# Kernel optimization log

Measured on AMD Instinct MI355X. Metric: run time of the kernel, lower is better.

The kernel has to match this reference:

```python
import jax, jax.numpy as jnp
import numpy as np

N_USERS = 8192
D = 128
E = 262144        # known edges (nonzero_idx rows)
K = 131072        # static pad size for data-dependent candidate extraction
COS_THR = 0.3
TAU = 0.2


def setup_inputs() -> dict:
    key = jax.random.key(0)
    k1, k2, k3, k4 = jax.random.split(key, 4)
    user_emb = jax.random.normal(k1, (N_USERS, D), dtype=jnp.float32)
    nonzero_idx = jax.random.randint(k2, (E, 2), 0, N_USERS)
    W = jax.random.normal(k3, (2, 2 * D), dtype=jnp.float32) * 0.05  # mlp_s weight [2, 2*latent]
    b = jnp.zeros((2,), dtype=jnp.float32)                            # mlp_s bias
    gumbel_noise = jax.random.gumbel(k4, (E + K, 2), dtype=jnp.float32)
    return {"user_emb": user_emb, "W": W, "b": b,
            "gumbel_noise": gumbel_noise, "nonzero_idx": nonzero_idx}


def reference(user_emb, W, b, gumbel_noise, nonzero_idx):
    n = user_emb.shape[0]
    # ---- get_candidate_pair ----
    norm = jnp.linalg.norm(user_emb, axis=1, keepdims=True)
    u = user_emb / jnp.maximum(norm, 1e-12)          # F.normalize(dim=1)
    cos = u @ u.T                                    # [n, n]
    diag = jnp.arange(n)
    cos = cos.at[diag, diag].set(-1.0)               # fill_diagonal_(-1)
    cos = cos.at[nonzero_idx[:, 0], nonzero_idx[:, 1]].set(-1.0)
    mask = cos > COS_THR
    # static-size nonzero; padded slots point at (0,0) where cos == -1,
    # so they behave as invalid candidates (weight 0 downstream).
    ci, cj = jnp.nonzero(mask, size=K, fill_value=0)
    cand_vals = cos[ci, cj]                          # padded entries = -1
    cand_idx = jnp.stack([ci, cj], axis=1)           # [K, 2]

    # ---- forward ----
    pair_idx = jnp.concatenate([nonzero_idx, cand_idx], axis=0)   # [E+K, 2]
    u_emb = user_emb[pair_idx[:, 0]]
    v_emb = user_emb[pair_idx[:, 1]]
    concat_emb = jnp.concatenate([u_emb, v_emb], axis=1)          # [E+K, 2D]
    logits = concat_emb @ W.T + b                                 # [E+K, 2]

    # hard gumbel-softmax (straight-through)
    y_soft = jax.nn.softmax((logits + gumbel_noise) / TAU, axis=-1)
    y_hard = jax.nn.one_hot(jnp.argmax(y_soft, axis=-1), 2, dtype=y_soft.dtype)
    gumbel_output = y_hard + y_soft - jax.lax.stop_gradient(y_soft)
    gumbel_retain = gumbel_output[:, 0]                           # [E+K]

    # ---- get_edge_weight ----
    cand_w = jnp.maximum(cand_vals, 0.0)                          # masked_fill(<0, 0)
    weights = jnp.concatenate([jnp.ones((E,), dtype=cand_w.dtype), cand_w])
    w = gumbel_retain * weights                                   # [E+K]
    gumbel_01 = w
    gumbel_retain_w = jnp.concatenate([w[:, None], w[:, None]], axis=0)  # [2(E+K), 1]
    return gumbel_01, gumbel_retain_w, pair_idx
```

## Files before the change

kernel.cpp:

```cpp
#include <hip/hip_runtime.h>
#include <hip/hip_bf16.h>
#include <math.h>

#define N_USERS 8192
#define DIMS    128
#define EDGES   262144
#define KCAND   131072
#define NTOT    (EDGES + KCAND)
#define LISTCAP 131072
#define CAPB    512
#define NTILES  2080
#define COS_THR 0.3f
#define EPS_SEL 6e-3f
#define LOGIT_MARGIN 2e-3f
#define DEADKEY 0xFFFFFFFFu

typedef short bf16x8 __attribute__((ext_vector_type(8)));
typedef float f32x4  __attribute__((ext_vector_type(4)));


__global__ __launch_bounds__(256) void prep_k(const float* __restrict__ x,
                                              const float* __restrict__ W,
                                              const int* __restrict__ nz,
                                              float* __restrict__ un,
                                              unsigned short* __restrict__ u0,
                                              float4* __restrict__ P,
                                              unsigned* __restrict__ excl) {
  if (blockIdx.x < 256) {
#pragma clang fp contract(off)
    const int tid  = threadIdx.x;
    const int rloc = tid >> 3;
    const int j    = tid & 7;
    const int i    = blockIdx.x * 32 + rloc;
    const float* r = x + (size_t)i * DIMS;

    float vals[16];
    float a = 0.f;
#pragma unroll
    for (int b8 = 0; b8 < 16; ++b8) {
      float t = r[b8 * 8 + j];
      vals[b8] = t;
      a = a + t * t;
    }
    a = a + __shfl_xor(a, 1, 64);
    a = a + __shfl_xor(a, 2, 64);
    float s = a + __shfl_xor(a, 4, 64);
    float n = (float)sqrt((double)s);
    n = fmaxf(n, 1e-12f);

    unsigned short* slab = u0 + (size_t)(i >> 7) * 16384 + (i & 127) * 8;
    float p0 = 0.f, p1 = 0.f, p2 = 0.f, p3 = 0.f;
#pragma unroll
    for (int b8 = 0; b8 < 16; ++b8) {
      int k = b8 * 8 + j;
      float t = vals[b8];
      float v = t / n;
      un[(size_t)i * DIMS + k] = v;
      __hip_bfloat16 h = __float2bfloat16(v);
      slab[(size_t)b8 * 1024 + j] = *(unsigned short*)&h;
      p0 = fmaf(t, W[k], p0);
      p1 = fmaf(t, W[128 + k], p1);
      p2 = fmaf(t, W[256 + k], p2);
      p3 = fmaf(t, W[384 + k], p3);
    }
#pragma unroll
    for (int m = 1; m < 8; m <<= 1) {
      p0 += __shfl_xor(p0, m, 64);
      p1 += __shfl_xor(p1, m, 64);
      p2 += __shfl_xor(p2, m, 64);
      p3 += __shfl_xor(p3, m, 64);
    }
    if (j == 0) P[i] = make_float4(p0, p1, p2, p3);
  } else {
    int t = (blockIdx.x - 256) * 256 + threadIdx.x;
    if (t < EDGES) {
      uint2 e = ((const uint2*)nz)[t];
      atomicOr(&excl[(size_t)e.x * 256 + (e.y >> 5)], 1u << (e.y & 31));
    }
  }
}

__global__ __launch_bounds__(512) void mfma_pass(const unsigned short* __restrict__ u0,
                                                 uint2* __restrict__ list,
                                                 int* __restrict__ gcount) {
  __shared__ uint2 svec[CAPB];
  __shared__ int lcnt, lbase;

  const int tid  = threadIdx.x;
  const int lane = tid & 63;
  const int wv   = tid >> 6;
  const int quad = lane >> 4;
  const int l15  = lane & 15;

  int rem = blockIdx.x, bi = 0;
  while (rem >= 64 - bi) { rem -= 64 - bi; ++bi; }
  const int bj = bi + rem;
  const int I0 = bi * 128, J0 = bj * 128;
  const int moff = (wv & 3) * 32, noff = (wv >> 2) * 64;

  if (tid == 0) lcnt = 0;
  __syncthreads();

  const unsigned short* __restrict__ Abase = u0 + (size_t)bi * 16384;
  const unsigned short* __restrict__ Bbase = u0 + (size_t)bj * 16384;

  bf16x8 af[4][2], bfr[4][4];
#pragma unroll
  for (int kc = 0; kc < 4; ++kc) {
    const int cq = kc * 4 + quad;
#pragma unroll
    for (int mt = 0; mt < 2; ++mt)
      af[kc][mt] = *(const bf16x8*)&Abase[(size_t)(cq * 128 + moff + mt * 16 + l15) * 8];
#pragma unroll
    for (int nt = 0; nt < 4; ++nt)
      bfr[kc][nt] = *(const bf16x8*)&Bbase[(size_t)(cq * 128 + noff + nt * 16 + l15) * 8];
  }

  f32x4 acc[2][4];
#pragma unroll
  for (int mt = 0; mt < 2; ++mt)
#pragma unroll
    for (int nt = 0; nt < 4; ++nt)
#pragma unroll
      for (int g = 0; g < 4; ++g) acc[mt][nt][g] = 0.f;

#pragma unroll
  for (int kc = 0; kc < 4; ++kc)
#pragma unroll
    for (int mt = 0; mt < 2; ++mt)
#pragma unroll
      for (int nt = 0; nt < 4; ++nt)
        acc[mt][nt] = __builtin_amdgcn_mfma_f32_16x16x32_bf16(
            af[kc][mt], bfr[kc][nt], acc[mt][nt], 0, 0, 0);

#pragma unroll
  for (int mt = 0; mt < 2; ++mt)
#pragma unroll
    for (int nt = 0; nt < 4; ++nt)
#pragma unroll
      for (int g = 0; g < 4; ++g) {
        float v = acc[mt][nt][g];
        if (v > COS_THR - EPS_SEL) {
          int i = I0 + moff + mt * 16 + quad * 4 + g;
          int j = J0 + noff + nt * 16 + l15;
          if (j > i) {
            int idx = atomicAdd(&lcnt, 2);
            if (idx + 1 < CAPB) {
              svec[idx]     = make_uint2(((unsigned)i << 13) | j,
                                         __float_as_uint(v));
              svec[idx + 1] = make_uint2(((unsigned)j << 13) | i,
                                         __float_as_uint(v));
            }
          }
        }
      }

  __syncthreads();
  int n = min(lcnt, CAPB);
  if (tid == 0) lbase = atomicAdd(gcount, n);
  __syncthreads();
  int base = lbase;
  for (int t = tid; t < n; t += 512) {
    int o = base + t;
    if (o < LISTCAP) list[o] = svec[t];
  }
}

__global__ __launch_bounds__(256) void resolve_hist_k(const float* __restrict__ un,
                                                      const unsigned* __restrict__ excl,
                                                      uint2* __restrict__ list,
                                                      const int* __restrict__ gcount,
                                                      int* __restrict__ row_cnt) {
  int t = blockIdx.x * 256 + threadIdx.x;
  int n = min(*gcount, LISTCAP);
  if (t >= n) return;
  uint2 e = list[t];
  int i = e.x >> 13, j = e.x & 8191;
  unsigned word = excl[(size_t)i * 256 + (j >> 5)];
  bool alive = !((word >> (j & 31)) & 1u);
  float v = __uint_as_float(e.y);
  if (alive && v <= COS_THR + EPS_SEL) {
    const float* a = un + (size_t)i * DIMS;
    const float* b = un + (size_t)j * DIMS;
    float s = 0.f;
    for (int k = 0; k < DIMS; ++k) s = fmaf(a[k], b[k], s);
    alive = (s > COS_THR);
    if (alive) list[t] = make_uint2(e.x, __float_as_uint(s));
  }
  if (!alive) list[t] = make_uint2(DEADKEY, 0u);
  else        atomicAdd(&row_cnt[i], 1);
}

__global__ __launch_bounds__(256) void scan8k(const int* __restrict__ cnt,
                                              int* __restrict__ off) {
  __shared__ int sm[256];
  int t = threadIdx.x;
  int base = t * 32;
  int s = 0;
  for (int i = 0; i < 32; ++i) s += cnt[base + i];
  sm[t] = s;
  __syncthreads();
  int x = s;
  for (int d = 1; d < 256; d <<= 1) {
    int y = (t >= d) ? sm[t - d] : 0;
    __syncthreads();
    x += y;
    sm[t] = x;
    __syncthreads();
  }
  int run = x - s;
  for (int i = 0; i < 32; ++i) { off[base + i] = run; run += cnt[base + i]; }
  if (t == 255) off[N_USERS] = x;
}

__global__ __launch_bounds__(256) void scatter_k(const uint2* __restrict__ list,
                                                 const int* __restrict__ gcount,
                                                 const int* __restrict__ row_off,
                                                 int* __restrict__ row_pos,
                                                 int* __restrict__ cand_i,
                                                 int* __restrict__ cand_j,
                                                 float* __restrict__ cand_v) {
  int t = blockIdx.x * 256 + threadIdx.x;
  int n = min(*gcount, LISTCAP);
  if (t >= n) return;
  uint2 e = list[t];
  if (e.x == DEADKEY) return;
  int i = e.x >> 13, j = e.x & 8191;
  int pos = row_off[i] + atomicAdd(&row_pos[i], 1);
  if (pos < KCAND) {
    cand_i[pos] = i;
    cand_j[pos] = j;
    cand_v[pos] = __uint_as_float(e.y);
  }
}

__global__ __launch_bounds__(256) void sortrow_k(const int* __restrict__ row_off,
                                                 const int* __restrict__ row_cnt,
                                                 int* __restrict__ cand_j,
                                                 float* __restrict__ cand_v) {
  int r = blockIdx.x * 256 + threadIdx.x;
  if (r >= N_USERS) return;
  int o = row_off[r], c = row_cnt[r];
  if (o + c > KCAND) c = max(0, KCAND - o);
  for (int a = 1; a < c; ++a) {
    int jv = cand_j[o + a];
    float vv = cand_v[o + a];
    int b = a - 1;
    while (b >= 0 && cand_j[o + b] > jv) {
      cand_j[o + b + 1] = cand_j[o + b];
      cand_v[o + b + 1] = cand_v[o + b];
      --b;
    }
    cand_j[o + b + 1] = jv;
    cand_v[o + b + 1] = vv;
  }
}

__global__ __launch_bounds__(256) void finalize_k(const float* __restrict__ ue,
                                                  const float* __restrict__ W,
                                                  const float* __restrict__ b,
                                                  const float* __restrict__ g,
                                                  const int* __restrict__ nz,
                                                  const int* __restrict__ cand_i,
                                                  const int* __restrict__ cand_j,
                                                  const float* __restrict__ cand_v,
                                                  const int* __restrict__ row_off,
                                                  const float4* __restrict__ P,
                                                  float* __restrict__ out) {
  int p = blockIdx.x * 256 + threadIdx.x;
  if (p >= NTOT) return;

  int i, j;
  float wgt;
  if (p < EDGES) {
    i = nz[2 * p];
    j = nz[2 * p + 1];
    wgt = 1.0f;
  } else {
    int q = p - EDGES;
    if (q >= row_off[N_USERS]) {
      out[p] = 0.0f;
      out[NTOT + p] = 0.0f;
      out[2 * NTOT + p] = 0.0f;
      out[3 * NTOT + 2 * p + 0] = 0.0f;
      out[3 * NTOT + 2 * p + 1] = 0.0f;
      return;
    }
    i = cand_i[q];
    j = cand_j[q];
    wgt = fmaxf(cand_v[q], 0.0f);
  }

  float4 Pi = P[i], Pj = P[j];
  float l0 = Pi.x + Pj.y + b[0];
  float l1 = Pi.z + Pj.w + b[1];
  float g0 = g[2 * p], g1 = g[2 * p + 1];
  float s0 = l0 + g0, s1 = l1 + g1;

  if (fabsf(s0 - s1) < LOGIT_MARGIN) {
    const float* ri = ue + (size_t)i * DIMS;
    const float* rj = ue + (size_t)j * DIMS;
    float e0 = 0.f, e1 = 0.f;
    for (int k = 0; k < DIMS; ++k) {
      e0 = fmaf(ri[k], W[k], e0);
      e1 = fmaf(ri[k], W[256 + k], e1);
    }
    for (int k = 0; k < DIMS; ++k) {
      e0 = fmaf(rj[k], W[128 + k], e0);
      e1 = fmaf(rj[k], W[384 + k], e1);
    }
    s0 = (e0 + b[0]) + g0;
    s1 = (e1 + b[1]) + g1;
  }

  float w = (s0 >= s1) ? wgt : 0.0f;

  out[p] = w;
  out[NTOT + p] = w;
  out[2 * NTOT + p] = w;
  out[3 * NTOT + 2 * p + 0] = (float)i;
  out[3 * NTOT + 2 * p + 1] = (float)j;
}

extern "C" void kernel_launch(void* const* d_in, const int* in_sizes, int n_in,
                              void* d_out, int out_size, void* d_ws, size_t ws_size,
                              hipStream_t stream) {
  (void)in_sizes; (void)n_in; (void)out_size; (void)ws_size;

  const float* user_emb = (const float*)d_in[0];
  const float* W        = (const float*)d_in[1];
  const float* b        = (const float*)d_in[2];
  const float* gnoise   = (const float*)d_in[3];
  const int*   nz       = (const int*)d_in[4];
  float* out = (float*)d_out;

  char* ws = (char*)d_ws;
  float*          un      = (float*)(ws + 0);
  unsigned short* u0      = (unsigned short*)(ws + (4u << 20));
  unsigned*       excl    = (unsigned*)(ws + (6u << 20));
  char*           zbase   = ws + (14u << 20);
  int*            gcount  = (int*)(zbase);
  int*            row_cnt = (int*)(zbase + 64);
  int*            row_pos = (int*)(zbase + 64 + 32768);
  int*            row_off = (int*)(ws + (14u << 20) + (96u << 10));
  uint2*          list    = (uint2*)(ws + (15u << 20));
  int*            cand_i  = (int*)(ws + (16u << 20));
  int*            cand_j  = (int*)(ws + (16u << 20) + (512u << 10));
  float*          cand_v  = (float*)(ws + (17u << 20));
  float4*         P       = (float4*)(ws + (17u << 20) + (512u << 10));

  hipMemsetAsync(excl, 0, (8u << 20) + (96u << 10), stream);

  prep_k<<<256 + EDGES / 256, 256, 0, stream>>>(user_emb, W, nz, un, u0, P, excl);
  mfma_pass<<<NTILES, 512, 0, stream>>>(u0, list, gcount);
  resolve_hist_k<<<LISTCAP / 256, 256, 0, stream>>>(un, excl, list, gcount,
                                                    row_cnt);
  scan8k<<<1, 256, 0, stream>>>(row_cnt, row_off);
  scatter_k<<<LISTCAP / 256, 256, 0, stream>>>(list, gcount, row_off, row_pos,
                                               cand_i, cand_j, cand_v);
  sortrow_k<<<N_USERS / 256, 256, 0, stream>>>(row_off, row_cnt, cand_j, cand_v);
  finalize_k<<<NTOT / 256, 256, 0, stream>>>(user_emb, W, b, gnoise, nz,
                                             cand_i, cand_j, cand_v, row_off,
                                             P, out);
}
```

Measured before the change: 150.5 us.

## Enlarge cosine tiles to 128x256 and double-buffer fragment loads

The upper-triangle cosine pass now has each block cover a 128-row by 256-column tile, with every wave owning 128 columns, which roughly halves the number of blocks. Fragment loads for the four K-chunks are split into two register buffers so the next chunk's loads can overlap the current MFMAs. The per-block candidate buffer is doubled to match the larger tile. The cost is higher register pressure from 16 accumulator tiles plus two fragment sets, and diagonal tiles where part of the work is wasted.

```diff
diff --git a/kernel.cpp b/kernel.cpp
--- a/kernel.cpp
+++ b/kernel.cpp
@@ -8,8 +8,8 @@
 #define KCAND   131072
 #define NTOT    (EDGES + KCAND)
 #define LISTCAP 131072
-#define CAPB    512
-#define NTILES  2080
+#define CAPB    1024
+#define NTILES  1056
 #define COS_THR 0.3f
 #define EPS_SEL 6e-3f
 #define LOGIT_MARGIN 2e-3f
@@ -92,57 +92,87 @@
   const int quad = lane >> 4;
   const int l15  = lane & 15;
 
-  int rem = blockIdx.x, bi = 0;
-  while (rem >= 64 - bi) { rem -= 64 - bi; ++bi; }
-  const int bj = bi + rem;
-  const int I0 = bi * 128, J0 = bj * 128;
-  const int moff = (wv & 3) * 32, noff = (wv >> 2) * 64;
+  int b = blockIdx.x, cj = 0;
+  while ((cj + 1) * (cj + 2) <= b) ++cj;
+  const int ri = b - cj * (cj + 1);
+  const int I0 = ri * 128, J0 = cj * 256;
+  const int moff = (wv & 3) * 32;
+  const int nhalf = wv >> 2;
+  const int jbase = J0 + nhalf * 128;
 
   if (tid == 0) lcnt = 0;
   __syncthreads();
 
-  const unsigned short* __restrict__ Abase = u0 + (size_t)bi * 16384;
-  const unsigned short* __restrict__ Bbase = u0 + (size_t)bj * 16384;
-
-  bf16x8 af[4][2], bfr[4][4];
-#pragma unroll
-  for (int kc = 0; kc < 4; ++kc) {
-    const int cq = kc * 4 + quad;
-#pragma unroll
-    for (int mt = 0; mt < 2; ++mt)
-      af[kc][mt] = *(const bf16x8*)&Abase[(size_t)(cq * 128 + moff + mt * 16 + l15) * 8];
-#pragma unroll
-    for (int nt = 0; nt < 4; ++nt)
-      bfr[kc][nt] = *(const bf16x8*)&Bbase[(size_t)(cq * 128 + noff + nt * 16 + l15) * 8];
-  }
-
-  f32x4 acc[2][4];
+  const unsigned short* __restrict__ Abase = u0 + (size_t)ri * 16384;
+  const unsigned short* __restrict__ Bbase = u0 + (size_t)(cj * 2 + nhalf) * 16384;
+
+  f32x4 acc[2][8];
 #pragma unroll
   for (int mt = 0; mt < 2; ++mt)
 #pragma unroll
-    for (int nt = 0; nt < 4; ++nt)
+    for (int nt = 0; nt < 8; ++nt)
 #pragma unroll
       for (int g = 0; g < 4; ++g) acc[mt][nt][g] = 0.f;
 
-#pragma unroll
-  for (int kc = 0; kc < 4; ++kc)
-#pragma unroll
-    for (int mt = 0; mt < 2; ++mt)
-#pragma unroll
-      for (int nt = 0; nt < 4; ++nt)
-        acc[mt][nt] = __builtin_amdgcn_mfma_f32_16x16x32_bf16(
-            af[kc][mt], bfr[kc][nt], acc[mt][nt], 0, 0, 0);
+  bf16x8 a0_0, a0_1, b0_0, b0_1, b0_2, b0_3, b0_4, b0_5, b0_6, b0_7;
+  bf16x8 a1_0, a1_1, b1_0, b1_1, b1_2, b1_3, b1_4, b1_5, b1_6, b1_7;
+
+#define LOADF(AN0, AN1, BN0, BN1, BN2, BN3, BN4, BN5, BN6, BN7, KC)           \
+  {                                                                           \
+    const int cq = (KC) * 4 + quad;                                           \
+    AN0 = *(const bf16x8*)&Abase[(size_t)(cq * 128 + moff + l15) * 8];        \
+    AN1 = *(const bf16x8*)&Abase[(size_t)(cq * 128 + moff + 16 + l15) * 8];   \
+    BN0 = *(const bf16x8*)&Bbase[(size_t)(cq * 128 + 0 * 16 + l15) * 8];      \
+    BN1 = *(const bf16x8*)&Bbase[(size_t)(cq * 128 + 1 * 16 + l15) * 8];      \
+    BN2 = *(const bf16x8*)&Bbase[(size_t)(cq * 128 + 2 * 16 + l15) * 8];      \
+    BN3 = *(const bf16x8*)&Bbase[(size_t)(cq * 128 + 3 * 16 + l15) * 8];      \
+    BN4 = *(const bf16x8*)&Bbase[(size_t)(cq * 128 + 4 * 16 + l15) * 8];      \
+    BN5 = *(const bf16x8*)&Bbase[(size_t)(cq * 128 + 5 * 16 + l15) * 8];      \
+    BN6 = *(const bf16x8*)&Bbase[(size_t)(cq * 128 + 6 * 16 + l15) * 8];      \
+    BN7 = *(const bf16x8*)&Bbase[(size_t)(cq * 128 + 7 * 16 + l15) * 8];      \
+  }
+
+#define MFMAF(AN0, AN1, BN0, BN1, BN2, BN3, BN4, BN5, BN6, BN7)               \
+  {                                                                           \
+    acc[0][0] = __builtin_amdgcn_mfma_f32_16x16x32_bf16(AN0, BN0, acc[0][0], 0, 0, 0); \
+    acc[0][1] = __builtin_amdgcn_mfma_f32_16x16x32_bf16(AN0, BN1, acc[0][1], 0, 0, 0); \
+    acc[0][2] = __builtin_amdgcn_mfma_f32_16x16x32_bf16(AN0, BN2, acc[0][2], 0, 0, 0); \
+    acc[0][3] = __builtin_amdgcn_mfma_f32_16x16x32_bf16(AN0, BN3, acc[0][3], 0, 0, 0); \
+    acc[0][4] = __builtin_amdgcn_mfma_f32_16x16x32_bf16(AN0, BN4, acc[0][4], 0, 0, 0); \
+    acc[0][5] = __builtin_amdgcn_mfma_f32_16x16x32_bf16(AN0, BN5, acc[0][5], 0, 0, 0); \
+    acc[0][6] = __builtin_amdgcn_mfma_f32_16x16x32_bf16(AN0, BN6, acc[0][6], 0, 0, 0); \
+    acc[0][7] = __builtin_amdgcn_mfma_f32_16x16x32_bf16(AN0, BN7, acc[0][7], 0, 0, 0); \
+    acc[1][0] = __builtin_amdgcn_mfma_f32_16x16x32_bf16(AN1, BN0, acc[1][0], 0, 0, 0); \
+    acc[1][1] = __builtin_amdgcn_mfma_f32_16x16x32_bf16(AN1, BN1, acc[1][1], 0, 0, 0); \
+    acc[1][2] = __builtin_amdgcn_mfma_f32_16x16x32_bf16(AN1, BN2, acc[1][2], 0, 0, 0); \
+    acc[1][3] = __builtin_amdgcn_mfma_f32_16x16x32_bf16(AN1, BN3, acc[1][3], 0, 0, 0); \
+    acc[1][4] = __builtin_amdgcn_mfma_f32_16x16x32_bf16(AN1, BN4, acc[1][4], 0, 0, 0); \
+    acc[1][5] = __builtin_amdgcn_mfma_f32_16x16x32_bf16(AN1, BN5, acc[1][5], 0, 0, 0); \
+    acc[1][6] = __builtin_amdgcn_mfma_f32_16x16x32_bf16(AN1, BN6, acc[1][6], 0, 0, 0); \
+    acc[1][7] = __builtin_amdgcn_mfma_f32_16x16x32_bf16(AN1, BN7, acc[1][7], 0, 0, 0); \
+  }
+
+  LOADF(a0_0, a0_1, b0_0, b0_1, b0_2, b0_3, b0_4, b0_5, b0_6, b0_7, 0)
+  LOADF(a1_0, a1_1, b1_0, b1_1, b1_2, b1_3, b1_4, b1_5, b1_6, b1_7, 1)
+  MFMAF(a0_0, a0_1, b0_0, b0_1, b0_2, b0_3, b0_4, b0_5, b0_6, b0_7)
+  LOADF(a0_0, a0_1, b0_0, b0_1, b0_2, b0_3, b0_4, b0_5, b0_6, b0_7, 2)
+  MFMAF(a1_0, a1_1, b1_0, b1_1, b1_2, b1_3, b1_4, b1_5, b1_6, b1_7)
+  LOADF(a1_0, a1_1, b1_0, b1_1, b1_2, b1_3, b1_4, b1_5, b1_6, b1_7, 3)
+  MFMAF(a0_0, a0_1, b0_0, b0_1, b0_2, b0_3, b0_4, b0_5, b0_6, b0_7)
+  MFMAF(a1_0, a1_1, b1_0, b1_1, b1_2, b1_3, b1_4, b1_5, b1_6, b1_7)
+#undef LOADF
+#undef MFMAF
 
 #pragma unroll
   for (int mt = 0; mt < 2; ++mt)
 #pragma unroll
-    for (int nt = 0; nt < 4; ++nt)
+    for (int nt = 0; nt < 8; ++nt)
 #pragma unroll
       for (int g = 0; g < 4; ++g) {
         float v = acc[mt][nt][g];
         if (v > COS_THR - EPS_SEL) {
           int i = I0 + moff + mt * 16 + quad * 4 + g;
-          int j = J0 + noff + nt * 16 + l15;
+          int j = jbase + nt * 16 + l15;
           if (j > i) {
             int idx = atomicAdd(&lcnt, 2);
             if (idx + 1 < CAPB) {
```

New measurement: 148.5 us. About the same (-1.4%).

## Use 256x256 upper-triangle tiles with LDS staging in the cosine MFMA pass

Applied to the files above, without the earlier changes.

The similarity kernel now uses 256x256 output tiles over the upper triangle, giving 528 blocks of 1024 threads instead of 2080 blocks of 128x128. Both operand panels are staged cooperatively into shared memory, and each wave reads its 64x64 fragments from LDS. This cuts redundant global and L2 reads of the bf16 embeddings and per-block overhead. In exchange it uses much more LDS per block (operand tiles plus a larger candidate buffer), so occupancy may drop, and fewer blocks may leave compute units idle.

```diff
diff --git a/kernel.cpp b/kernel.cpp
--- a/kernel.cpp
+++ b/kernel.cpp
@@ -8,8 +8,8 @@
 #define KCAND   131072
 #define NTOT    (EDGES + KCAND)
 #define LISTCAP 131072
-#define CAPB    512
-#define NTILES  2080
+#define CAPB    2048
+#define NTILES  528
 #define COS_THR 0.3f
 #define EPS_SEL 6e-3f
 #define LOGIT_MARGIN 2e-3f
@@ -80,9 +80,11 @@
   }
 }
 
-__global__ __launch_bounds__(512) void mfma_pass(const unsigned short* __restrict__ u0,
-                                                 uint2* __restrict__ list,
-                                                 int* __restrict__ gcount) {
+__global__ __launch_bounds__(1024) void mfma_pass(const unsigned short* __restrict__ u0,
+                                                  uint2* __restrict__ list,
+                                                  int* __restrict__ gcount) {
+  __shared__ __align__(16) unsigned short As[2][16][128][8];
+  __shared__ __align__(16) unsigned short Bs[2][16][128][8];
   __shared__ uint2 svec[CAPB];
   __shared__ int lcnt, lbase;
 
@@ -91,58 +93,74 @@
   const int wv   = tid >> 6;
   const int quad = lane >> 4;
   const int l15  = lane & 15;
-
-  int rem = blockIdx.x, bi = 0;
-  while (rem >= 64 - bi) { rem -= 64 - bi; ++bi; }
-  const int bj = bi + rem;
-  const int I0 = bi * 128, J0 = bj * 128;
-  const int moff = (wv & 3) * 32, noff = (wv >> 2) * 64;
+  const int wm   = wv >> 2;
+  const int wn   = wv & 3;
+
+  int rem = blockIdx.x, cj = 0;
+  while (rem >= cj + 1) { rem -= cj + 1; ++cj; }
+  const int ri = rem;
+  const int I0 = ri * 256, J0 = cj * 256;
 
   if (tid == 0) lcnt = 0;
+
+  const uint4* __restrict__ Asrc = (const uint4*)(u0 + (size_t)ri * 32768);
+  const uint4* __restrict__ Bsrc = (const uint4*)(u0 + (size_t)cj * 32768);
+  uint4* Ad = (uint4*)As;
+  uint4* Bd = (uint4*)Bs;
+  {
+    uint4 pA[4], pB[4];
+#pragma unroll
+    for (int it = 0; it < 4; ++it) {
+      pA[it] = Asrc[it * 1024 + tid];
+      pB[it] = Bsrc[it * 1024 + tid];
+    }
+#pragma unroll
+    for (int it = 0; it < 4; ++it) {
+      Ad[it * 1024 + tid] = pA[it];
+      Bd[it * 1024 + tid] = pB[it];
+    }
+  }
   __syncthreads();
 
-  const unsigned short* __restrict__ Abase = u0 + (size_t)bi * 16384;
-  const unsigned short* __restrict__ Bbase = u0 + (size_t)bj * 16384;
-
-  bf16x8 af[4][2], bfr[4][4];
+  f32x4 acc[4][4];
+#pragma unroll
+  for (int mt = 0; mt < 4; ++mt)
+#pragma unroll
+    for (int nt = 0; nt < 4; ++nt)
+#pragma unroll
+      for (int g = 0; g < 4; ++g) acc[mt][nt][g] = 0.f;
+
+  const int aslab = wm >> 1, arow0 = (wm & 1) * 64;
+  const int bslab = wn >> 1, brow0 = (wn & 1) * 64;
+
 #pragma unroll
   for (int kc = 0; kc < 4; ++kc) {
     const int cq = kc * 4 + quad;
-#pragma unroll
-    for (int mt = 0; mt < 2; ++mt)
-      af[kc][mt] = *(const bf16x8*)&Abase[(size_t)(cq * 128 + moff + mt * 16 + l15) * 8];
+    bf16x8 af[4], bf[4];
+#pragma unroll
+    for (int mt = 0; mt < 4; ++mt)
+      af[mt] = *(const bf16x8*)&As[aslab][cq][arow0 + mt * 16 + l15][0];
 #pragma unroll
     for (int nt = 0; nt < 4; ++nt)
-      bfr[kc][nt] = *(const bf16x8*)&Bbase[(size_t)(cq * 128 + noff + nt * 16 + l15) * 8];
-  }
-
-  f32x4 acc[2][4];
-#pragma unroll
-  for (int mt = 0; mt < 2; ++mt)
-#pragma unroll
-    for (int nt = 0; nt < 4; ++nt)
-#pragma unroll
-      for (int g = 0; g < 4; ++g) acc[mt][nt][g] = 0.f;
-
-#pragma unroll
-  for (int kc = 0; kc < 4; ++kc)
-#pragma unroll
-    for (int mt = 0; mt < 2; ++mt)
+      bf[nt] = *(const bf16x8*)&Bs[bslab][cq][brow0 + nt * 16 + l15][0];
+#pragma unroll
+    for (int mt = 0; mt < 4; ++mt)
 #pragma unroll
       for (int nt = 0; nt < 4; ++nt)
         acc[mt][nt] = __builtin_amdgcn_mfma_f32_16x16x32_bf16(
-            af[kc][mt], bfr[kc][nt], acc[mt][nt], 0, 0, 0);
-
-#pragma unroll
-  for (int mt = 0; mt < 2; ++mt)
+            af[mt], bf[nt], acc[mt][nt], 0, 0, 0);
+  }
+
+#pragma unroll
+  for (int mt = 0; mt < 4; ++mt)
 #pragma unroll
     for (int nt = 0; nt < 4; ++nt)
 #pragma unroll
       for (int g = 0; g < 4; ++g) {
         float v = acc[mt][nt][g];
         if (v > COS_THR - EPS_SEL) {
-          int i = I0 + moff + mt * 16 + quad * 4 + g;
-          int j = J0 + noff + nt * 16 + l15;
+          int i = I0 + wm * 64 + mt * 16 + quad * 4 + g;
+          int j = J0 + wn * 64 + nt * 16 + l15;
           if (j > i) {
             int idx = atomicAdd(&lcnt, 2);
             if (idx + 1 < CAPB) {
@@ -160,7 +178,7 @@
   if (tid == 0) lbase = atomicAdd(gcount, n);
   __syncthreads();
   int base = lbase;
-  for (int t = tid; t < n; t += 512) {
+  for (int t = tid; t < n; t += 1024) {
     int o = base + t;
     if (o < LISTCAP) list[o] = svec[t];
   }
@@ -352,7 +370,7 @@
   hipMemsetAsync(excl, 0, (8u << 20) + (96u << 10), stream);
 
   prep_k<<<256 + EDGES / 256, 256, 0, stream>>>(user_emb, W, nz, un, u0, P, excl);
-  mfma_pass<<<NTILES, 512, 0, stream>>>(u0, list, gcount);
+  mfma_pass<<<NTILES, 1024, 0, stream>>>(u0, list, gcount);
   resolve_hist_k<<<LISTCAP / 256, 256, 0, stream>>>(un, excl, list, gcount,
                                                     row_cnt);
   scan8k<<<1, 256, 0, stream>>>(row_cnt, row_off);
```

Result: faster. 139.2 us, median of 2 (-7.5%).
